# Kernel tuning notes

Measured on AMD Instinct MI355X. Metric: run time of the kernel, lower is better.

The kernel has to match this reference:

```python
import jax, jax.numpy as jnp
import numpy as np

B, C, H, W = 8, 128, 128, 128
D_MODEL = C
D_INNER = 2 * D_MODEL          # expand=2 -> 256
D_STATE = 64
HEADDIM = 32                   # _resolve_headdim(128, 32) -> 32
NHEADS = D_INNER // HEADDIM    # 8
D_CONV = 4
CHUNK = 64
GN_GROUPS = 8                  # _group_count(128, 8)
D_XBC = D_INNER + 2 * D_STATE  # 384
D_INPROJ = 2 * D_INNER + 2 * D_STATE + NHEADS  # 648


def _group_norm(x, g, b, groups=GN_GROUPS, eps=1e-5):
    Bn, Cn, Hh, Ww = x.shape
    xr = x.reshape(Bn, groups, Cn // groups, Hh, Ww)
    mu = xr.mean(axis=(2, 3, 4), keepdims=True)
    var = xr.var(axis=(2, 3, 4), keepdims=True)
    xr = (xr - mu) * jax.lax.rsqrt(var + eps)
    return xr.reshape(Bn, Cn, Hh, Ww) * g[None, :, None, None] + b[None, :, None, None]


def _grid_sample_bilinear_border(img, grid):
    # img: (B,C,H,W); grid: (B,H,W,2) with (x,y) in [-1,1]; align_corners=True, border padding
    _, _, Hh, Ww = img.shape
    gx = jnp.clip((grid[..., 0] + 1.0) * 0.5 * (Ww - 1), 0.0, Ww - 1.0)
    gy = jnp.clip((grid[..., 1] + 1.0) * 0.5 * (Hh - 1), 0.0, Hh - 1.0)
    x0 = jnp.floor(gx); y0 = jnp.floor(gy)
    wx = gx - x0; wy = gy - y0
    x0i = x0.astype(jnp.int32); y0i = y0.astype(jnp.int32)
    x1i = jnp.minimum(x0i + 1, Ww - 1); y1i = jnp.minimum(y0i + 1, Hh - 1)
    def per_b(im, y0b, y1b, x0b, x1b, wxb, wyb):
        v00 = im[:, y0b, x0b]; v01 = im[:, y0b, x1b]
        v10 = im[:, y1b, x0b]; v11 = im[:, y1b, x1b]
        return (v00 * (1 - wxb) + v01 * wxb) * (1 - wyb) + (v10 * (1 - wxb) + v11 * wxb) * wyb
    return jax.vmap(per_b)(img, y0i, y1i, x0i, x1i, wx, wy)


def _mamba(seq, in_proj_w, conv_w, conv_b, dt_bias, A_log, D_skip, norm_g, out_w):
    # seq: (Bs, L, d_model) -> (Bs, L, d_model); Mamba2/SSD-style selective scan
    Bs, L, _ = seq.shape
    pad = (CHUNK - L % CHUNK) % CHUNK
    if pad:
        seq = jnp.pad(seq, ((0, 0), (0, pad), (0, 0)))
    Lp = L + pad
    zxbcdt = jnp.einsum('bld,ed->ble', seq, in_proj_w)
    z = zxbcdt[..., :D_INNER]
    xBC = zxbcdt[..., D_INNER:D_INNER + D_XBC]
    dt = jax.nn.softplus(zxbcdt[..., -NHEADS:] + dt_bias)  # (Bs,Lp,nh)
    # causal depthwise conv1d, kernel D_CONV
    xp = jnp.pad(xBC, ((0, 0), (D_CONV - 1, 0), (0, 0)))
    xBC = sum(conv_w[:, k] * xp[:, k:k + Lp, :] for k in range(D_CONV)) + conv_b
    xBC = jax.nn.silu(xBC)
    xs = xBC[..., :D_INNER].reshape(Bs, Lp, NHEADS, HEADDIM)
    Bm = xBC[..., D_INNER:D_INNER + D_STATE]
    Cm = xBC[..., D_INNER + D_STATE:]
    A = -jnp.exp(A_log)  # (nh,)
    def step(h, inp):
        x_t, B_t, C_t, dt_t = inp  # (Bs,nh,hd),(Bs,ds),(Bs,ds),(Bs,nh)
        dA = jnp.exp(dt_t * A)  # (Bs,nh)
        h = h * dA[..., None, None] + (dt_t[..., None] * x_t)[..., None] * B_t[:, None, None, :]
        y = jnp.einsum('bhds,bs->bhd', h, C_t)
        return h, y
    h0 = jnp.zeros((Bs, NHEADS, HEADDIM, D_STATE), seq.dtype)
    _, ys = jax.lax.scan(step, h0, (jnp.moveaxis(xs, 1, 0), jnp.moveaxis(Bm, 1, 0), jnp.moveaxis(Cm, 1, 0), jnp.moveaxis(dt, 1, 0)))
    ys = jnp.moveaxis(ys, 0, 1) + D_skip[None, None, :, None] * xs  # (Bs,Lp,nh,hd)
    y = ys.reshape(Bs, Lp, D_INNER) * jax.nn.silu(z)  # gated
    y = y * jax.lax.rsqrt(jnp.mean(y * y, axis=-1, keepdims=True) + 1e-5) * norm_g  # RMSNorm
    out = jnp.einsum('ble,de->bld', y, out_w)
    return out[:, :L] if pad else out


def _forward(x, dw_w, gn_g, gn_b, pw_w, pw_b, in_proj_w, conv_w, conv_b, dt_bias, A_log, D_skip, norm_g, out_w):
    Bn, Cn, Hh, Ww = x.shape
    dn = ('NCHW', 'OIHW', 'NCHW')
    # offset_net: depthwise 5x5 -> GroupNorm -> GELU -> 1x1
    h1 = jax.lax.conv_general_dilated(x, dw_w, (1, 1), 'SAME', feature_group_count=Cn, dimension_numbers=dn)
    h1 = jax.nn.gelu(_group_norm(h1, gn_g, gn_b), approximate=False)
    off = jax.lax.conv_general_dilated(h1, pw_w, (1, 1), 'SAME', dimension_numbers=dn) + pw_b[None, :, None, None]
    offset = jnp.tanh(off) * min(8.0, max(Hh, Ww) * 0.1)  # (B,1,H,W)
    gy = jnp.linspace(-1.0, 1.0, Hh, dtype=x.dtype)
    gx = jnp.linspace(-1.0, 1.0, Ww, dtype=x.dtype)
    base_y, base_x = jnp.meshgrid(gy, gx, indexing='ij')  # (H,W)
    off_n = offset[:, 0] * (2.0 / max(Hh - 1, 1))  # horizontal scan: vertical offsets
    grid = jnp.stack([jnp.broadcast_to(base_x, (Bn, Hh, Ww)), jnp.clip(base_y + off_n, -1.0, 1.0)], axis=-1)
    deformed = _grid_sample_bilinear_border(x, grid)
    seq = deformed.transpose(0, 2, 3, 1).reshape(Bn * Hh, Ww, Cn)  # (b h) w c
    out = _mamba(seq, in_proj_w, conv_w, conv_b, dt_bias, A_log, D_skip, norm_g, out_w)
    out_2d = out.reshape(Bn, Hh, Ww, Cn).transpose(0, 3, 1, 2)
    return out_2d, offset


def setup_inputs() -> dict:
    key = jax.random.key(0)
    ks = jax.random.split(key, 8)
    return {
        'x': jax.random.normal(ks[0], (B, C, H, W), jnp.float32),
        'dw_w': jax.random.normal(ks[1], (C, 1, 5, 5), jnp.float32) * 0.05,
        'gn_g': jnp.ones((C,), jnp.float32),
        'gn_b': jnp.zeros((C,), jnp.float32),
        'pw_w': jax.random.normal(ks[2], (1, C, 1, 1), jnp.float32) * 0.02,
        'pw_b': jnp.zeros((1,), jnp.float32),
        'in_proj_w': jax.random.normal(ks[3], (D_INPROJ, D_MODEL), jnp.float32) * 0.02,
        'conv_w': jax.random.normal(ks[4], (D_XBC, D_CONV), jnp.float32) * 0.1,
        'conv_b': jnp.zeros((D_XBC,), jnp.float32),
        'dt_bias': jax.random.normal(ks[5], (NHEADS,), jnp.float32) * 0.1,
        'A_log': jnp.log(jnp.arange(1, NHEADS + 1, dtype=jnp.float32)),
        'D_skip': jnp.ones((NHEADS,), jnp.float32),
        'norm_g': jnp.ones((D_INNER,), jnp.float32),
        'out_w': jax.random.normal(ks[6], (D_MODEL, D_INNER), jnp.float32) * 0.02,
    }


def reference(x, dw_w, gn_g, gn_b, pw_w, pw_b, in_proj_w, conv_w, conv_b, dt_bias, A_log, D_skip, norm_g, out_w):
    return _forward(x, dw_w, gn_g, gn_b, pw_w, pw_b, in_proj_w, conv_w, conv_b, dt_bias, A_log, D_skip, norm_g, out_w)
```

## Files before the change

kernel.cpp:

```cpp
#include <hip/hip_runtime.h>
#include <math.h>


typedef _Float16 half8 __attribute__((ext_vector_type(8)));
typedef _Float16 half4 __attribute__((ext_vector_type(4)));
typedef float f32x4 __attribute__((ext_vector_type(4)));

__device__ __forceinline__ float b2f(unsigned short u) {
  return __uint_as_float(((unsigned int)u) << 16);
}
__device__ __forceinline__ bool in_is_f32(const void* gng) {
  return ((const unsigned int*)gng)[0] == 0x3F800000u;
}

#define P_DWW 0
#define P_CW 3200
#define P_CB 4736
#define P_GNG 5120
#define P_GNB 5248
#define P_PWW 5376
#define P_PWB 5504
#define P_DTB 5505
#define P_ALOG 5513
#define P_DSKIP 5521
#define P_NG 5529

__global__ void k_prep_all(const void* dww, const void* cw, const void* cb,
                           const void* gng, const void* gnb, const void* pww,
                           const void* pwb, const void* dtbias, const void* alog,
                           const void* dskip, const void* ng,
                           const void* wproj, const void* outw,
                           float* __restrict__ P, float* __restrict__ gst,
                           _Float16* __restrict__ wprojh, _Float16* __restrict__ outwh) {
  bool f = in_is_f32(gng);
  int stride = gridDim.x * blockDim.x;
  for (int i = blockIdx.x * blockDim.x + threadIdx.x; i < 98304; i += stride) {
    int row = i >> 7;
    float v = 0.f;
    if (row < 648) v = f ? ((const float*)wproj)[i] : b2f(((const unsigned short*)wproj)[i]);
    wprojh[i] = (_Float16)v;
  }
  for (int i = blockIdx.x * blockDim.x + threadIdx.x; i < 32768; i += stride) {
    int e = i & 255;
    float wv = f ? ((const float*)outw)[i] : b2f(((const unsigned short*)outw)[i]);
    float ngv = f ? ((const float*)ng)[e] : b2f(((const unsigned short*)ng)[e]);
    outwh[i] = (_Float16)(wv * ngv);
  }
  if (blockIdx.x == 0) {
    int tid = threadIdx.x;
    if (tid < 128) gst[tid] = 0.f;
    auto cvt = [&](const void* src, int n, int off) {
      for (int i = tid; i < n; i += 256)
        P[off + i] = f ? ((const float*)src)[i] : b2f(((const unsigned short*)src)[i]);
    };
    cvt(dww, 3200, P_DWW);
    cvt(cw, 1536, P_CW);
    cvt(cb, 384, P_CB);
    cvt(gng, 128, P_GNG);
    cvt(gnb, 128, P_GNB);
    cvt(pww, 128, P_PWW);
    cvt(pwb, 1, P_PWB);
    cvt(dtbias, 8, P_DTB);
    cvt(alog, 8, P_ALOG);
    cvt(dskip, 8, P_DSKIP);
    cvt(ng, 256, P_NG);
  }
}

__global__ __launch_bounds__(256) void k_dwconv_v6(const void* __restrict__ x,
                                                   const void* __restrict__ gng,
                                                   const float* __restrict__ P,
                                                   _Float16* __restrict__ h1h,
                                                   float* __restrict__ gst) {
  int bc = blockIdx.x;
  int b = bc >> 7, c = bc & 127;
  bool f32x = in_is_f32(gng);
  __shared__ float red[8];
  const float* xf = (const float*)x + (size_t)bc * 16384;
  const unsigned short* xb = (const unsigned short*)x + (size_t)bc * 16384;
  float w[25];
#pragma unroll
  for (int k = 0; k < 25; ++k) w[k] = P[P_DWW + c * 25 + k];

  int ox = (threadIdx.x & 31) * 4;
  int y0 = (threadIdx.x >> 5) * 16;
  float win[5][12];

  auto loadrow = [&](int gy, float* d) {
#pragma unroll
    for (int k = 0; k < 12; ++k) d[k] = 0.f;
    if (gy >= 0 && gy < 128) {
      if (f32x) {
        const float* rp = xf + gy * 128;
        if (ox >= 4) {
          float4 v = *(const float4*)(rp + ox - 4);
          d[0] = v.x; d[1] = v.y; d[2] = v.z; d[3] = v.w;
        }
        float4 v0 = *(const float4*)(rp + ox);
        d[4] = v0.x; d[5] = v0.y; d[6] = v0.z; d[7] = v0.w;
        if (ox < 124) {
          float4 v1 = *(const float4*)(rp + ox + 4);
          d[8] = v1.x; d[9] = v1.y; d[10] = v1.z; d[11] = v1.w;
        }
      } else {
        const unsigned short* rp = xb + gy * 128;
        if (ox >= 4) {
          ushort4 u = *(const ushort4*)(rp + ox - 4);
          d[0] = b2f(u.x); d[1] = b2f(u.y); d[2] = b2f(u.z); d[3] = b2f(u.w);
        }
        ushort4 u0 = *(const ushort4*)(rp + ox);
        d[4] = b2f(u0.x); d[5] = b2f(u0.y); d[6] = b2f(u0.z); d[7] = b2f(u0.w);
        if (ox < 124) {
          ushort4 u1 = *(const ushort4*)(rp + ox + 4);
          d[8] = b2f(u1.x); d[9] = b2f(u1.y); d[10] = b2f(u1.z); d[11] = b2f(u1.w);
        }
      }
    }
  };

#pragma unroll
  for (int i = 0; i < 4; ++i) loadrow(y0 - 2 + i, win[i]);

  float s = 0.f, sq = 0.f;
  _Float16* hp = h1h + (size_t)bc * 16384;
#pragma unroll
  for (int yo = 0; yo < 16; ++yo) {
    loadrow(y0 + yo + 2, win[(yo + 4) % 5]);
    float o4[4] = {0.f, 0.f, 0.f, 0.f};
#pragma unroll
    for (int ky = 0; ky < 5; ++ky) {
      const float* r = win[(yo + ky) % 5];
#pragma unroll
      for (int j = 0; j < 4; ++j)
#pragma unroll
        for (int kx = 0; kx < 5; ++kx)
          o4[j] += w[ky * 5 + kx] * r[j + kx + 2];
    }
    half4 oh;
#pragma unroll
    for (int j = 0; j < 4; ++j) {
      oh[j] = (_Float16)o4[j];
      s += o4[j]; sq += o4[j] * o4[j];
    }
    *(half4*)&hp[(y0 + yo) * 128 + ox] = oh;
  }

  for (int o = 32; o; o >>= 1) { s += __shfl_down(s, o, 64); sq += __shfl_down(sq, o, 64); }
  int wv = threadIdx.x >> 6;
  if ((threadIdx.x & 63) == 0) { red[wv] = s; red[4 + wv] = sq; }
  __syncthreads();
  if (threadIdx.x == 0) {
    float ts = red[0] + red[1] + red[2] + red[3];
    float tq = red[4] + red[5] + red[6] + red[7];
    int g = (b << 3) + (c >> 4);
    atomicAdd(&gst[g * 2], ts);
    atomicAdd(&gst[g * 2 + 1], tq);
  }
}

__global__ __launch_bounds__(256) void k_gn_part(const _Float16* __restrict__ h1h,
                                                 const float* __restrict__ gst,
                                                 const float* __restrict__ P,
                                                 float* __restrict__ part) {
  int bh2 = blockIdx.x;
  int b = bh2 >> 8;
  int h = (bh2 & 255) >> 1;
  int half = bh2 & 1;
  int tid = threadIdx.x;
  int w = tid & 127;
  int sub = tid >> 7;
  __shared__ float ls[8];
  __shared__ float sacc[2][128];
  if (tid < 4) {
    const float invN = 1.f / 262144.f;
    int g = b * 8 + half * 4 + tid;
    float mean = gst[g * 2] * invN;
    float var = gst[g * 2 + 1] * invN - mean * mean;
    ls[tid * 2] = mean;
    ls[tid * 2 + 1] = rsqrtf(var + 1e-5f);
  }
  __syncthreads();
  int cbase = half * 64 + sub * 32;
  const _Float16* hb = h1h + (((size_t)(b * 128 + cbase)) * 128 + h) * 128 + w;
  float acc = 0.f;
#pragma unroll 4
  for (int ci = 0; ci < 32; ++ci) {
    int c = cbase + ci;
    float v = (float)hb[(size_t)ci * 16384];
    int lg = (sub * 32 + ci) >> 4;
    float nv = (v - ls[lg * 2]) * ls[lg * 2 + 1] * P[P_GNG + c] + P[P_GNB + c];
    float ge = 0.5f * nv * (1.f + erff(nv * 0.70710678118f));
    acc += ge * P[P_PWW + c];
  }
  sacc[sub][w] = acc;
  __syncthreads();
  if (sub == 0) part[(size_t)bh2 * 128 + w] = acc + sacc[1][w];
}

__global__ __launch_bounds__(256) void k_deform_v5(const void* __restrict__ x,
                                                   const void* __restrict__ gng,
                                                   const float* __restrict__ part,
                                                   const float* __restrict__ P,
                                                   _Float16* __restrict__ seqc,
                                                   float* __restrict__ dout,
                                                   int s0) {
  int bh = s0 + blockIdx.x;
  int b = bh >> 7, h = bh & 127;
  int tid = threadIdx.x;
  int w = tid & 127;
  int half = tid >> 7;
  bool f32x = in_is_f32(gng);
  __shared__ float t[128 * 129];
  float ofv = tanhf(part[(size_t)bh * 256 + w] + part[(size_t)bh * 256 + 128 + w] +
                    P[P_PWB]) * 8.0f;
  if (half == 0) dout[16777216 + bh * 128 + w] = ofv;
  float gy = -1.f + (2.f / 127.f) * (float)h + ofv * (2.f / 127.f);
  gy = fminf(fmaxf(gy, -1.f), 1.f);
  float py = (gy + 1.f) * 0.5f * 127.f;
  py = fminf(fmaxf(py, 0.f), 127.f);
  float y0f = floorf(py);
  float wy = py - y0f;
  int y0 = (int)y0f;
  int y1 = min(y0 + 1, 127);
  const float* xfb = (const float*)x + (size_t)b * 128 * 16384;
  const unsigned short* xbb = (const unsigned short*)x + (size_t)b * 128 * 16384;
  int c0 = half * 64;
  for (int i = 0; i < 64; i += 2) {
    int ca = c0 + i, cb2 = c0 + i + 1;
    size_t a0 = (size_t)ca * 16384 + y0 * 128 + w;
    size_t a1 = (size_t)ca * 16384 + y1 * 128 + w;
    size_t b0 = (size_t)cb2 * 16384 + y0 * 128 + w;
    size_t b1 = (size_t)cb2 * 16384 + y1 * 128 + w;
    float va0, va1, vb0, vb1;
    if (f32x) { va0 = xfb[a0]; va1 = xfb[a1]; vb0 = xfb[b0]; vb1 = xfb[b1]; }
    else      { va0 = b2f(xbb[a0]); va1 = b2f(xbb[a1]);
                vb0 = b2f(xbb[b0]); vb1 = b2f(xbb[b1]); }
    t[ca * 129 + w] = va0 + wy * (va1 - va0);
    t[cb2 * 129 + w] = vb0 + wy * (vb1 - vb0);
  }
  __syncthreads();
  int c2 = tid & 127;
  int lb = (tid >> 7) * 64;
  _Float16* sp = seqc + (size_t)blockIdx.x * 16384;
  for (int i = 0; i < 64; ++i) {
    int l = lb + i;
    sp[l * 128 + c2] = (_Float16)t[c2 * 129 + l];
  }
}

__global__ __launch_bounds__(512) void k_gemm1_v8(const _Float16* __restrict__ seqh,
                                                  const _Float16* __restrict__ wprojh,
                                                  const float* __restrict__ P,
                                                  _Float16* __restrict__ zh,
                                                  _Float16* __restrict__ xch,
                                                  float* __restrict__ dtb) {
  __shared__ __align__(16) _Float16 lds[33792];
  _Float16* lA = lds;
  _Float16* lB = lds + 8192;
  int m0 = blockIdx.x * 128;
  int e0 = blockIdx.y * 256;
  int tid = threadIdx.x;
  int lane = tid & 63;
  int wv = tid >> 6;
  int grp = tid >> 8;
  int wvl = wv & 3;
  int rsel = lane & 15, q = lane >> 4;
  bool isz = (e0 == 0);
  bool isdt = (e0 == 512) && (grp == 1);

  f32x4 acc[2][8];
#pragma unroll
  for (int rf = 0; rf < 2; ++rf)
#pragma unroll
    for (int cf = 0; cf < 8; ++cf) acc[rf][cf] = (f32x4){0.f, 0.f, 0.f, 0.f};

  for (int k0 = 0; k0 < 128; k0 += 64) {
    if (k0) __syncthreads();
#pragma unroll
    for (int p = 0; p < 2; ++p) {
      int idx = tid + 512 * p;
      int row = idx >> 3, ch = idx & 7;
      int dch = ch ^ (row & 7);
      *(half8*)&lA[row * 64 + dch * 8] =
          *(const half8*)&seqh[(size_t)(m0 + row) * 128 + k0 + ch * 8];
    }
#pragma unroll
    for (int p = 0; p < 4; ++p) {
      int idx = tid + 512 * p;
      int row = idx >> 3, ch = idx & 7;
      int dch = ch ^ (row & 7);
      *(half8*)&lB[row * 64 + dch * 8] =
          *(const half8*)&wprojh[(size_t)(e0 + row) * 128 + k0 + ch * 8];
    }
    __syncthreads();
#pragma unroll
    for (int kk = 0; kk < 2; ++kk) {
      half8 a[2];
#pragma unroll
      for (int rf = 0; rf < 2; ++rf) {
        int row = wvl * 32 + rf * 16 + rsel;
        int ch = (kk * 4 + q) ^ (row & 7);
        a[rf] = *(const half8*)&lA[row * 64 + ch * 8];
      }
#pragma unroll
      for (int cf = 0; cf < 8; ++cf) {
        if (isdt && cf > 0) continue;
        int row = grp * 128 + cf * 16 + rsel;
        int ch = (kk * 4 + q) ^ (row & 7);
        half8 b = *(const half8*)&lB[row * 64 + ch * 8];
        acc[0][cf] = __builtin_amdgcn_mfma_f32_16x16x32_f16(a[0], b, acc[0][cf], 0, 0, 0);
        acc[1][cf] = __builtin_amdgcn_mfma_f32_16x16x32_f16(a[1], b, acc[1][cf], 0, 0, 0);
      }
    }
  }

  __syncthreads();
  _Float16* sx = lds + grp * 16896;
  if (!isz && !isdt) {
#pragma unroll
    for (int rf = 0; rf < 2; ++rf) {
#pragma unroll
      for (int r = 0; r < 4; ++r) {
        int row = wvl * 32 + rf * 16 + q * 4 + r;
#pragma unroll
        for (int cf = 0; cf < 8; ++cf)
          sx[row * 132 + cf * 16 + rsel] = (_Float16)acc[rf][cf][r];
      }
    }
  }
  __syncthreads();

  if (isz) {
#pragma unroll
    for (int rf = 0; rf < 2; ++rf) {
      int mb = m0 + wvl * 32 + rf * 16 + q * 4;
#pragma unroll
      for (int cf = 0; cf < 8; ++cf) {
        _Float16* pz = zh + (size_t)mb * 256 + grp * 128 + cf * 16 + rsel;
#pragma unroll
        for (int r = 0; r < 4; ++r) pz[(size_t)r * 256] = (_Float16)acc[rf][cf][r];
      }
    }
  } else if (isdt) {
#pragma unroll
    for (int rf = 0; rf < 2; ++rf) {
      int mb = m0 + wvl * 32 + rf * 16 + q * 4;
      if (rsel < 8) {
        float bias = P[P_DTB + rsel];
#pragma unroll
        for (int r = 0; r < 4; ++r) {
          float dv = acc[rf][0][r] + bias;
          float sp = (dv > 20.f) ? dv : log1pf(__expf(dv));
          dtb[(size_t)(mb + r) * 8 + rsel] = sp;
        }
      }
    }
  } else {
    int tg = tid & 255;
    int cc = tg & 127;
    int rh = tg >> 7;
    int eg = (e0 - 256) + grp * 128 + cc;
    float w0 = P[P_CW + eg * 4 + 0], w1 = P[P_CW + eg * 4 + 1];
    float w2 = P[P_CW + eg * 4 + 2], w3 = P[P_CW + eg * 4 + 3];
    float bb = P[P_CB + eg];
    int r0 = rh * 64;
    float x0 = (r0 >= 3) ? (float)sx[(r0 - 3) * 132 + cc] : 0.f;
    float x1 = (r0 >= 2) ? (float)sx[(r0 - 2) * 132 + cc] : 0.f;
    float x2 = (r0 >= 1) ? (float)sx[(r0 - 1) * 132 + cc] : 0.f;
    _Float16* xo = xch + (size_t)m0 * 384 + eg;
    for (int r = r0; r < r0 + 64; ++r) {
      float x3 = (float)sx[r * 132 + cc];
      float a = bb + w0 * x0 + w1 * x1 + w2 * x2 + w3 * x3;
      xo[(size_t)r * 384] = (_Float16)(a * __builtin_amdgcn_rcpf(1.f + __expf(-a)));
      x0 = x1; x1 = x2; x2 = x3;
    }
  }
}

__global__ __launch_bounds__(256) void k_ssd_v4(const _Float16* __restrict__ xch,
                                                const _Float16* __restrict__ zh,
                                                const float* __restrict__ dtb,
                                                const float* __restrict__ P,
                                                _Float16* __restrict__ ys,
                                                float* __restrict__ rr) {
  int seq = blockIdx.x;
  int tid = threadIdx.x;
  int lane = tid & 63, wv = tid >> 6;
  int rsel = lane & 15, q = lane >> 4;
  __shared__ __align__(16) _Float16 G[128 * 128];
  __shared__ __align__(16) _Float16 Xt[32 * 128];
  __shared__ float dts[128 * 8];
  __shared__ float Ts[8 * 128];
  __shared__ float ejs[128];
  const _Float16* xb = xch + (size_t)seq * 49152;
  const _Float16* zb = zh + (size_t)seq * 32768;
  const float* dtp = dtb + (size_t)seq * 1024;

  for (int i = tid; i < 1024; i += 256) dts[i] = dtp[i];
  __syncthreads();
  if (tid < 8) {
    float a = 0.f;
    for (int l = 0; l < 128; ++l) { a += dts[l * 8 + tid]; Ts[tid * 128 + l] = a; }
  }

  f32x4 gacc[2][8];
#pragma unroll
  for (int rf = 0; rf < 2; ++rf)
#pragma unroll
    for (int cf = 0; cf < 8; ++cf) gacc[rf][cf] = (f32x4){0.f, 0.f, 0.f, 0.f};
#pragma unroll
  for (int kk = 0; kk < 2; ++kk) {
    half8 a[2];
#pragma unroll
    for (int rf = 0; rf < 2; ++rf) {
      int l = wv * 32 + rf * 16 + rsel;
      a[rf] = *(const half8*)&xb[(size_t)l * 384 + 320 + kk * 32 + q * 8];
    }
#pragma unroll
    for (int cf = 0; cf < 8; ++cf) {
      int j = cf * 16 + rsel;
      half8 b = *(const half8*)&xb[(size_t)j * 384 + 256 + kk * 32 + q * 8];
      gacc[0][cf] = __builtin_amdgcn_mfma_f32_16x16x32_f16(a[0], b, gacc[0][cf], 0, 0, 0);
      gacc[1][cf] = __builtin_amdgcn_mfma_f32_16x16x32_f16(a[1], b, gacc[1][cf], 0, 0, 0);
    }
  }
#pragma unroll
  for (int rf = 0; rf < 2; ++rf) {
#pragma unroll
    for (int r = 0; r < 4; ++r) {
      int l = wv * 32 + rf * 16 + q * 4 + r;
#pragma unroll
      for (int cf = 0; cf < 8; ++cf) {
        int j = cf * 16 + rsel;
        G[l * 128 + (((j >> 3) ^ (l & 7)) << 3) + (j & 7)] = (_Float16)gacc[rf][cf][r];
      }
    }
  }
  __syncthreads();

  float ssq[2][4];
#pragma unroll
  for (int rf = 0; rf < 2; ++rf)
#pragma unroll
    for (int r = 0; r < 4; ++r) ssq[rf][r] = 0.f;

  _Float16* yp = ys + (size_t)seq * 32768;
  for (int h = 0; h < 8; ++h) {
    float Ah = -__expf(P[P_ALOG + h]);
    float Dk = P[P_DSKIP + h];
    {
      int j = tid >> 1, ds = (tid & 1) * 16;
      float dtj = dts[j * 8 + h];
      half8 v0 = *(const half8*)&xb[(size_t)j * 384 + h * 32 + ds];
      half8 v1 = *(const half8*)&xb[(size_t)j * 384 + h * 32 + ds + 8];
#pragma unroll
      for (int e = 0; e < 8; ++e) {
        int d0 = ds + e, d1 = ds + 8 + e;
        Xt[d0 * 128 + (((j >> 3) ^ (d0 & 7)) << 3) + (j & 7)] = (_Float16)((float)v0[e] * dtj);
        Xt[d1 * 128 + (((j >> 3) ^ (d1 & 7)) << 3) + (j & 7)] = (_Float16)((float)v1[e] * dtj);
      }
      if (tid < 128) {
        float TE = Ts[h * 128 + ((tid >> 5) << 5) + 31];
        ejs[tid] = __expf(Ah * (TE - Ts[h * 128 + tid]));
      }
    }
    __syncthreads();
    f32x4 acc[2][2];
#pragma unroll
    for (int rf = 0; rf < 2; ++rf)
#pragma unroll
      for (int cf = 0; cf < 2; ++cf) acc[rf][cf] = (f32x4){0.f, 0.f, 0.f, 0.f};
#pragma unroll
    for (int kk = 0; kk < 4; ++kk) {
      if (kk <= wv) {
        int jb = kk * 32 + q * 8;
        int chk = kk * 4 + q;
        half8 a[2];
        if (kk == wv) {
          float4 tj0 = *(const float4*)&Ts[h * 128 + jb];
          float4 tj1 = *(const float4*)&Ts[h * 128 + jb + 4];
          float tj[8] = {tj0.x, tj0.y, tj0.z, tj0.w, tj1.x, tj1.y, tj1.z, tj1.w};
#pragma unroll
          for (int rf = 0; rf < 2; ++rf) {
            int l = wv * 32 + rf * 16 + rsel;
            half8 g = *(const half8*)&G[l * 128 + ((chk ^ (l & 7)) << 3)];
            float Tl = Ts[h * 128 + l];
            half8 w;
#pragma unroll
            for (int e = 0; e < 8; ++e) {
              int j = jb + e;
              float m = (j <= l) ? __expf(Ah * (Tl - tj[e])) : 0.f;
              w[e] = (_Float16)((float)g[e] * m);
            }
            a[rf] = w;
          }
        } else {
          float TE = Ts[h * 128 + kk * 32 + 31];
          float4 e0v = *(const float4*)&ejs[jb];
          float4 e1v = *(const float4*)&ejs[jb + 4];
          float ej[8] = {e0v.x, e0v.y, e0v.z, e0v.w, e1v.x, e1v.y, e1v.z, e1v.w};
#pragma unroll
          for (int rf = 0; rf < 2; ++rf) {
            int l = wv * 32 + rf * 16 + rsel;
            half8 g = *(const half8*)&G[l * 128 + ((chk ^ (l & 7)) << 3)];
            float el = __expf(Ah * (Ts[h * 128 + l] - TE));
            half8 w;
#pragma unroll
            for (int e = 0; e < 8; ++e)
              w[e] = (_Float16)((float)g[e] * el * ej[e]);
            a[rf] = w;
          }
        }
#pragma unroll
        for (int cf = 0; cf < 2; ++cf) {
          int d = cf * 16 + rsel;
          half8 b = *(const half8*)&Xt[d * 128 + ((chk ^ (d & 7)) << 3)];
          acc[0][cf] = __builtin_amdgcn_mfma_f32_16x16x32_f16(a[0], b, acc[0][cf], 0, 0, 0);
          acc[1][cf] = __builtin_amdgcn_mfma_f32_16x16x32_f16(a[1], b, acc[1][cf], 0, 0, 0);
        }
      }
    }
#pragma unroll
    for (int rf = 0; rf < 2; ++rf) {
      int lb = wv * 32 + rf * 16 + q * 4;
#pragma unroll
      for (int cf = 0; cf < 2; ++cf) {
        int d = cf * 16 + rsel;
#pragma unroll
        for (int r = 0; r < 4; ++r) {
          int l = lb + r;
          float xv = (float)xb[(size_t)l * 384 + h * 32 + d];
          float zv = (float)zb[(size_t)l * 256 + h * 32 + d];
          float y = acc[rf][cf][r] + Dk * xv;
          float yg = y * (zv / (1.f + __expf(-zv)));
          ssq[rf][r] += yg * yg;
          yp[(size_t)l * 256 + h * 32 + d] = (_Float16)yg;
        }
      }
    }
    __syncthreads();
  }

  float* rp = rr + (size_t)seq * 128;
#pragma unroll
  for (int rf = 0; rf < 2; ++rf) {
#pragma unroll
    for (int r = 0; r < 4; ++r) {
      float ss = ssq[rf][r];
      ss += __shfl_xor(ss, 1, 64);
      ss += __shfl_xor(ss, 2, 64);
      ss += __shfl_xor(ss, 4, 64);
      ss += __shfl_xor(ss, 8, 64);
      if (rsel == 0) rp[wv * 32 + rf * 16 + q * 4 + r] = rsqrtf(ss * (1.f / 256.f) + 1e-5f);
    }
  }
}

__global__ __launch_bounds__(256) void k_gemm2_v4(const _Float16* __restrict__ ysg,
                                                  const float* __restrict__ rr,
                                                  const _Float16* __restrict__ outwh,
                                                  float* __restrict__ dout,
                                                  int tok0) {
  __shared__ __align__(16) _Float16 lA[128 * 64];
  __shared__ __align__(16) _Float16 lB[64 * 64];
  int t0 = blockIdx.x * 64;
  int tid = threadIdx.x;
  int lane = tid & 63;
  int wv = tid >> 6;
  f32x4 acc[2][4];
#pragma unroll
  for (int rf = 0; rf < 2; ++rf)
#pragma unroll
    for (int cf = 0; cf < 4; ++cf) acc[rf][cf] = (f32x4){0.f, 0.f, 0.f, 0.f};

  int rsel = lane & 15, q = lane >> 4;
  for (int k0 = 0; k0 < 256; k0 += 64) {
    if (k0) __syncthreads();
#pragma unroll
    for (int p = 0; p < 4; ++p) {
      int idx = tid + 256 * p;
      int row = idx >> 3, ch = idx & 7;
      int dch = ch ^ (row & 7);
      *(half8*)&lA[row * 64 + dch * 8] =
          *(const half8*)&outwh[(size_t)row * 256 + k0 + ch * 8];
    }
#pragma unroll
    for (int p = 0; p < 2; ++p) {
      int idx = tid + 256 * p;
      int row = idx >> 3, ch = idx & 7;
      int dch = ch ^ (row & 7);
      float rv = rr[t0 + row];
      half8 v = *(const half8*)&ysg[(size_t)(t0 + row) * 256 + k0 + ch * 8];
      half8 o;
#pragma unroll
      for (int e = 0; e < 8; ++e) o[e] = (_Float16)((float)v[e] * rv);
      *(half8*)&lB[row * 64 + dch * 8] = o;
    }
    __syncthreads();
#pragma unroll
    for (int kk = 0; kk < 2; ++kk) {
      half8 a[2];
#pragma unroll
      for (int rf = 0; rf < 2; ++rf) {
        int row = wv * 32 + rf * 16 + rsel;
        int ch = (kk * 4 + q) ^ (row & 7);
        a[rf] = *(const half8*)&lA[row * 64 + ch * 8];
      }
#pragma unroll
      for (int cf = 0; cf < 4; ++cf) {
        int row = cf * 16 + rsel;
        int ch = (kk * 4 + q) ^ (row & 7);
        half8 b = *(const half8*)&lB[row * 64 + ch * 8];
        acc[0][cf] = __builtin_amdgcn_mfma_f32_16x16x32_f16(a[0], b, acc[0][cf], 0, 0, 0);
        acc[1][cf] = __builtin_amdgcn_mfma_f32_16x16x32_f16(a[1], b, acc[1][cf], 0, 0, 0);
      }
    }
  }

  int l0 = tok0 + t0;
  int b = l0 >> 14;
  int rem0 = l0 & 16383;
#pragma unroll
  for (int rf = 0; rf < 2; ++rf) {
    int cbase = wv * 32 + rf * 16 + q * 4;
#pragma unroll
    for (int cf = 0; cf < 4; ++cf) {
#pragma unroll
      for (int r = 0; r < 4; ++r) {
        dout[(size_t)(b * 128 + cbase + r) * 16384 + rem0 + cf * 16 + rsel] = acc[rf][cf][r];
      }
    }
  }
}

extern "C" void kernel_launch(void* const* d_in, const int* in_sizes, int n_in,
                              void* d_out, int out_size, void* d_ws, size_t ws_size,
                              hipStream_t stream) {
  const void* x      = d_in[0];
  const void* dww    = d_in[1];
  const void* gng    = d_in[2];
  const void* gnb    = d_in[3];
  const void* pww    = d_in[4];
  const void* pwb    = d_in[5];
  const void* wproj  = d_in[6];
  const void* cw     = d_in[7];
  const void* cb     = d_in[8];
  const void* dtbias = d_in[9];
  const void* alog   = d_in[10];
  const void* dskip  = d_in[11];
  const void* ng     = d_in[12];
  const void* outw   = d_in[13];
  float* out = (float*)d_out;

  char* ws = (char*)d_ws;
  float* gst        = (float*)(ws + 0);
  float* P          = (float*)(ws + 8192);
  _Float16* wprojh  = (_Float16*)(ws + 40960);
  _Float16* outwh   = (_Float16*)(ws + 372736);
  float* part       = (float*)(ws + 503808);
  char* cbase       = ws + 1552384;

  _Float16* h1h = (_Float16*)out;

  const int opts[11] = {1024, 512, 256, 128, 64, 32, 16, 8, 4, 2, 1};
  int CH = 1;
  for (int i = 0; i < 11; ++i) {
    if (1552384ull + (unsigned long long)opts[i] * 266752ull <= (unsigned long long)ws_size) {
      CH = opts[i];
      break;
    }
  }
  int NC = 1024 / CH;

  _Float16* seqh = (_Float16*)(cbase);
  _Float16* zh   = (_Float16*)(cbase + (size_t)CH * 32768);
  _Float16* xch  = (_Float16*)(cbase + (size_t)CH * 98304);
  float* dtbf    = (float*)(cbase + (size_t)CH * 196608);
  _Float16* ysh  = (_Float16*)(cbase + (size_t)CH * 200704);
  float* rrf     = (float*)(cbase + (size_t)CH * 266240);

  k_prep_all<<<128, 256, 0, stream>>>(dww, cw, cb, gng, gnb, pww, pwb, dtbias,
                                      alog, dskip, ng, wproj, outw, P, gst,
                                      wprojh, outwh);
  k_dwconv_v6<<<1024, 256, 0, stream>>>(x, gng, P, h1h, gst);
  k_gn_part<<<2048, 256, 0, stream>>>(h1h, gst, P, part);

  int M = CH * 128;
  for (int c = 0; c < NC; ++c) {
    int s0 = c * CH;
    k_deform_v5<<<CH, 256, 0, stream>>>(x, gng, part, P, seqh, out, s0);
    k_gemm1_v8<<<dim3(M / 128, 3), 512, 0, stream>>>(seqh, wprojh, P, zh, xch, dtbf);
    k_ssd_v4<<<CH, 256, 0, stream>>>(xch, zh, dtbf, P, ysh, rrf);
    k_gemm2_v4<<<dim3(M / 64), 256, 0, stream>>>(ysh, rrf, outwh, out, s0 * 128);
  }
}
```

Baseline: 449.3 us.

## Split SSD heads across two wave groups with 512-thread blocks

The SSD kernel now runs 512 threads per sequence block. Two groups of four waves each handle four of the eight heads, each group with its own Xt and ejs buffers, and the initial C·B^T Gram matrix is split across all eight waves. Per-row sum-of-squares partials from the two groups are combined through shared memory (reusing Ts) before the RMS scale is written. This halves the serial head loop per block and adds parallelism, at the cost of more shared memory and register pressure per block, which may lower occupancy.

```diff
diff --git a/kernel.cpp b/kernel.cpp
--- a/kernel.cpp
+++ b/kernel.cpp
@@ -377,7 +377,7 @@
   }
 }
 
-__global__ __launch_bounds__(256) void k_ssd_v4(const _Float16* __restrict__ xch,
+__global__ __launch_bounds__(512) void k_ssd_v5(const _Float16* __restrict__ xch,
                                                 const _Float16* __restrict__ zh,
                                                 const float* __restrict__ dtb,
                                                 const float* __restrict__ P,
@@ -386,53 +386,47 @@
   int seq = blockIdx.x;
   int tid = threadIdx.x;
   int lane = tid & 63, wv = tid >> 6;
+  int grp = wv >> 2, wvl = wv & 3;
+  int tg = tid & 255;
   int rsel = lane & 15, q = lane >> 4;
   __shared__ __align__(16) _Float16 G[128 * 128];
-  __shared__ __align__(16) _Float16 Xt[32 * 128];
+  __shared__ __align__(16) _Float16 Xt[2][32 * 128];
   __shared__ float dts[128 * 8];
   __shared__ float Ts[8 * 128];
-  __shared__ float ejs[128];
+  __shared__ float ejs[2][128];
   const _Float16* xb = xch + (size_t)seq * 49152;
   const _Float16* zb = zh + (size_t)seq * 32768;
   const float* dtp = dtb + (size_t)seq * 1024;
 
-  for (int i = tid; i < 1024; i += 256) dts[i] = dtp[i];
+  for (int i = tid; i < 1024; i += 512) dts[i] = dtp[i];
   __syncthreads();
   if (tid < 8) {
     float a = 0.f;
     for (int l = 0; l < 128; ++l) { a += dts[l * 8 + tid]; Ts[tid * 128 + l] = a; }
   }
 
-  f32x4 gacc[2][8];
-#pragma unroll
-  for (int rf = 0; rf < 2; ++rf)
-#pragma unroll
-    for (int cf = 0; cf < 8; ++cf) gacc[rf][cf] = (f32x4){0.f, 0.f, 0.f, 0.f};
-#pragma unroll
-  for (int kk = 0; kk < 2; ++kk) {
-    half8 a[2];
-#pragma unroll
-    for (int rf = 0; rf < 2; ++rf) {
-      int l = wv * 32 + rf * 16 + rsel;
-      a[rf] = *(const half8*)&xb[(size_t)l * 384 + 320 + kk * 32 + q * 8];
-    }
-#pragma unroll
-    for (int cf = 0; cf < 8; ++cf) {
-      int j = cf * 16 + rsel;
-      half8 b = *(const half8*)&xb[(size_t)j * 384 + 256 + kk * 32 + q * 8];
-      gacc[0][cf] = __builtin_amdgcn_mfma_f32_16x16x32_f16(a[0], b, gacc[0][cf], 0, 0, 0);
-      gacc[1][cf] = __builtin_amdgcn_mfma_f32_16x16x32_f16(a[1], b, gacc[1][cf], 0, 0, 0);
-    }
-  }
-#pragma unroll
-  for (int rf = 0; rf < 2; ++rf) {
-#pragma unroll
-    for (int r = 0; r < 4; ++r) {
-      int l = wv * 32 + rf * 16 + q * 4 + r;
+  {
+    f32x4 gacc[8];
+#pragma unroll
+    for (int cf = 0; cf < 8; ++cf) gacc[cf] = (f32x4){0.f, 0.f, 0.f, 0.f};
+#pragma unroll
+    for (int kk = 0; kk < 2; ++kk) {
+      int l = wv * 16 + rsel;
+      half8 a = *(const half8*)&xb[(size_t)l * 384 + 320 + kk * 32 + q * 8];
 #pragma unroll
       for (int cf = 0; cf < 8; ++cf) {
         int j = cf * 16 + rsel;
-        G[l * 128 + (((j >> 3) ^ (l & 7)) << 3) + (j & 7)] = (_Float16)gacc[rf][cf][r];
+        half8 b = *(const half8*)&xb[(size_t)j * 384 + 256 + kk * 32 + q * 8];
+        gacc[cf] = __builtin_amdgcn_mfma_f32_16x16x32_f16(a, b, gacc[cf], 0, 0, 0);
+      }
+    }
+#pragma unroll
+    for (int r = 0; r < 4; ++r) {
+      int l = wv * 16 + q * 4 + r;
+#pragma unroll
+      for (int cf = 0; cf < 8; ++cf) {
+        int j = cf * 16 + rsel;
+        G[l * 128 + (((j >> 3) ^ (l & 7)) << 3) + (j & 7)] = (_Float16)gacc[cf][r];
       }
     }
   }
@@ -445,23 +439,26 @@
     for (int r = 0; r < 4; ++r) ssq[rf][r] = 0.f;
 
   _Float16* yp = ys + (size_t)seq * 32768;
-  for (int h = 0; h < 8; ++h) {
+  for (int hh = 0; hh < 4; ++hh) {
+    int h = grp * 4 + hh;
     float Ah = -__expf(P[P_ALOG + h]);
     float Dk = P[P_DSKIP + h];
     {
-      int j = tid >> 1, ds = (tid & 1) * 16;
+      int j = tg >> 1, ds = (tg & 1) * 16;
       float dtj = dts[j * 8 + h];
       half8 v0 = *(const half8*)&xb[(size_t)j * 384 + h * 32 + ds];
       half8 v1 = *(const half8*)&xb[(size_t)j * 384 + h * 32 + ds + 8];
 #pragma unroll
       for (int e = 0; e < 8; ++e) {
         int d0 = ds + e, d1 = ds + 8 + e;
-        Xt[d0 * 128 + (((j >> 3) ^ (d0 & 7)) << 3) + (j & 7)] = (_Float16)((float)v0[e] * dtj);
-        Xt[d1 * 128 + (((j >> 3) ^ (d1 & 7)) << 3) + (j & 7)] = (_Float16)((float)v1[e] * dtj);
-      }
-      if (tid < 128) {
-        float TE = Ts[h * 128 + ((tid >> 5) << 5) + 31];
-        ejs[tid] = __expf(Ah * (TE - Ts[h * 128 + tid]));
+        Xt[grp][d0 * 128 + (((j >> 3) ^ (d0 & 7)) << 3) + (j & 7)] =
+            (_Float16)((float)v0[e] * dtj);
+        Xt[grp][d1 * 128 + (((j >> 3) ^ (d1 & 7)) << 3) + (j & 7)] =
+            (_Float16)((float)v1[e] * dtj);
+      }
+      if (tg < 128) {
+        float TE = Ts[h * 128 + ((tg >> 5) << 5) + 31];
+        ejs[grp][tg] = __expf(Ah * (TE - Ts[h * 128 + tg]));
       }
     }
     __syncthreads();
@@ -472,17 +469,17 @@
       for (int cf = 0; cf < 2; ++cf) acc[rf][cf] = (f32x4){0.f, 0.f, 0.f, 0.f};
 #pragma unroll
     for (int kk = 0; kk < 4; ++kk) {
-      if (kk <= wv) {
+      if (kk <= wvl) {
         int jb = kk * 32 + q * 8;
         int chk = kk * 4 + q;
         half8 a[2];
-        if (kk == wv) {
+        if (kk == wvl) {
           float4 tj0 = *(const float4*)&Ts[h * 128 + jb];
           float4 tj1 = *(const float4*)&Ts[h * 128 + jb + 4];
           float tj[8] = {tj0.x, tj0.y, tj0.z, tj0.w, tj1.x, tj1.y, tj1.z, tj1.w};
 #pragma unroll
           for (int rf = 0; rf < 2; ++rf) {
-            int l = wv * 32 + rf * 16 + rsel;
+            int l = wvl * 32 + rf * 16 + rsel;
             half8 g = *(const half8*)&G[l * 128 + ((chk ^ (l & 7)) << 3)];
             float Tl = Ts[h * 128 + l];
             half8 w;
@@ -496,12 +493,12 @@
           }
         } else {
           float TE = Ts[h * 128 + kk * 32 + 31];
-          float4 e0v = *(const float4*)&ejs[jb];
-          float4 e1v = *(const float4*)&ejs[jb + 4];
+          float4 e0v = *(const float4*)&ejs[grp][jb];
+          float4 e1v = *(const float4*)&ejs[grp][jb + 4];
           float ej[8] = {e0v.x, e0v.y, e0v.z, e0v.w, e1v.x, e1v.y, e1v.z, e1v.w};
 #pragma unroll
           for (int rf = 0; rf < 2; ++rf) {
-            int l = wv * 32 + rf * 16 + rsel;
+            int l = wvl * 32 + rf * 16 + rsel;
             half8 g = *(const half8*)&G[l * 128 + ((chk ^ (l & 7)) << 3)];
             float el = __expf(Ah * (Ts[h * 128 + l] - TE));
             half8 w;
@@ -514,7 +511,7 @@
 #pragma unroll
         for (int cf = 0; cf < 2; ++cf) {
           int d = cf * 16 + rsel;
-          half8 b = *(const half8*)&Xt[d * 128 + ((chk ^ (d & 7)) << 3)];
+          half8 b = *(const half8*)&Xt[grp][d * 128 + ((chk ^ (d & 7)) << 3)];
           acc[0][cf] = __builtin_amdgcn_mfma_f32_16x16x32_f16(a[0], b, acc[0][cf], 0, 0, 0);
           acc[1][cf] = __builtin_amdgcn_mfma_f32_16x16x32_f16(a[1], b, acc[1][cf], 0, 0, 0);
         }
@@ -522,7 +519,7 @@
     }
 #pragma unroll
     for (int rf = 0; rf < 2; ++rf) {
-      int lb = wv * 32 + rf * 16 + q * 4;
+      int lb = wvl * 32 + rf * 16 + q * 4;
 #pragma unroll
       for (int cf = 0; cf < 2; ++cf) {
         int d = cf * 16 + rsel;
@@ -541,7 +538,6 @@
     __syncthreads();
   }
 
-  float* rp = rr + (size_t)seq * 128;
 #pragma unroll
   for (int rf = 0; rf < 2; ++rf) {
 #pragma unroll
@@ -551,8 +547,13 @@
       ss += __shfl_xor(ss, 2, 64);
       ss += __shfl_xor(ss, 4, 64);
       ss += __shfl_xor(ss, 8, 64);
-      if (rsel == 0) rp[wv * 32 + rf * 16 + q * 4 + r] = rsqrtf(ss * (1.f / 256.f) + 1e-5f);
-    }
+      if (rsel == 0) Ts[grp * 128 + wvl * 32 + rf * 16 + q * 4 + r] = ss;
+    }
+  }
+  __syncthreads();
+  if (tid < 128) {
+    float ss = Ts[tid] + Ts[128 + tid];
+    rr[(size_t)seq * 128 + tid] = rsqrtf(ss * (1.f / 256.f) + 1e-5f);
   }
 }
 
@@ -690,7 +691,7 @@
     int s0 = c * CH;
     k_deform_v5<<<CH, 256, 0, stream>>>(x, gng, part, P, seqh, out, s0);
     k_gemm1_v8<<<dim3(M / 128, 3), 512, 0, stream>>>(seqh, wprojh, P, zh, xch, dtbf);
-    k_ssd_v4<<<CH, 256, 0, stream>>>(xch, zh, dtbf, P, ysh, rrf);
+    k_ssd_v5<<<CH, 512, 0, stream>>>(xch, zh, dtbf, P, ysh, rrf);
     k_gemm2_v4<<<dim3(M / 64), 256, 0, stream>>>(ysh, rrf, outwh, out, s0 * 128);
   }
 }
```

Result: no change. 453.8 us (+1.0%).
